# Performance work log

Hardware: AMD Instinct MI355X
Metric: run time of the kernel (lower is better)

## Reference

```python
import jax, jax.numpy as jnp
import numpy as np

N_NODES = 100000
N_EDGES = 3200000
N_GRAPHS = 128
IN_DIM = 4
HID = 64
BN_EPS = 1e-5


def setup_inputs() -> dict:
    key = jax.random.key(0)
    ks = jax.random.split(key, 24)
    x = jax.random.normal(ks[0], (N_NODES, IN_DIM), dtype=jnp.float32)
    edge_index = jax.random.randint(ks[1], (2, N_EDGES), 0, N_NODES, dtype=jnp.int32)
    batch_ids = jnp.sort(jax.random.randint(ks[2], (N_NODES,), 0, N_GRAPHS, dtype=jnp.int32))

    def lin(k, out_d, in_d):
        s = 1.0 / np.sqrt(in_d)
        return jax.random.uniform(k, (out_d, in_d), jnp.float32, -s, s)

    inp = {
        'x': x, 'edge_index': edge_index, 'batch_ids': batch_ids,
        # SAGEConv i: out = lin_l(mean_neighbors) + lin_r(x_self); bias lives in lin_l
        'w1l': lin(ks[3], HID, IN_DIM), 'b1': jnp.zeros((HID,), jnp.float32), 'w1r': lin(ks[4], HID, IN_DIM),
        'bn1_g': jnp.ones((HID,), jnp.float32), 'bn1_b': jnp.zeros((HID,), jnp.float32),
        'w2l': lin(ks[5], HID, HID), 'b2': jnp.zeros((HID,), jnp.float32), 'w2r': lin(ks[6], HID, HID),
        'bn2_g': jnp.ones((HID,), jnp.float32), 'bn2_b': jnp.zeros((HID,), jnp.float32),
        'w3l': lin(ks[7], HID, HID), 'b3': jnp.zeros((HID,), jnp.float32), 'w3r': lin(ks[8], HID, HID),
        'bn3_g': jnp.ones((HID,), jnp.float32), 'bn3_b': jnp.zeros((HID,), jnp.float32),
        'fc1_w': lin(ks[9], 64, HID), 'fc1_b': jnp.zeros((64,), jnp.float32),
        'fc2_w': lin(ks[10], 2, 64), 'fc2_b': jnp.zeros((2,), jnp.float32),
    }
    return inp


def _sage(x, src, dst, deg_inv, wl, bl, wr):
    # mean-aggregate neighbor messages (source -> target), then two small GEMMs
    msum = jax.ops.segment_sum(x[src], dst, num_segments=N_NODES)  # [N, d]
    agg = msum * deg_inv[:, None]
    return agg @ wl.T + bl + x @ wr.T


def _bn(x, g, b):
    # BatchNorm1d in training mode: batch stats over node dim, biased variance
    m = jnp.mean(x, axis=0)
    v = jnp.mean((x - m) ** 2, axis=0)
    return (x - m) * jax.lax.rsqrt(v + BN_EPS) * g + b


def reference(x, edge_index, batch_ids,
              w1l, b1, w1r, bn1_g, bn1_b,
              w2l, b2, w2r, bn2_g, bn2_b,
              w3l, b3, w3r, bn3_g, bn3_b,
              fc1_w, fc1_b, fc2_w, fc2_b):
    src, dst = edge_index[0], edge_index[1]
    deg = jax.ops.segment_sum(jnp.ones((src.shape[0],), x.dtype), dst, num_segments=N_NODES)
    deg_inv = 1.0 / jnp.maximum(deg, 1.0)

    h = jax.nn.relu(_bn(_sage(x, src, dst, deg_inv, w1l, b1, w1r), bn1_g, bn1_b))
    h = jax.nn.relu(_bn(_sage(h, src, dst, deg_inv, w2l, b2, w2r), bn2_g, bn2_b))
    h = jax.nn.relu(_bn(_sage(h, src, dst, deg_inv, w3l, b3, w3r), bn3_g, bn3_b))

    # global_mean_pool over graphs
    gsum = jax.ops.segment_sum(h, batch_ids, num_segments=N_GRAPHS)
    gcnt = jax.ops.segment_sum(jnp.ones((h.shape[0],), h.dtype), batch_ids, num_segments=N_GRAPHS)
    pooled = gsum / jnp.maximum(gcnt, 1.0)[:, None]

    # MLP head (dropout = identity at inference)
    hid = jax.nn.relu(pooled @ fc1_w.T + fc1_b)
    return hid @ fc2_w.T + fc2_b
```

## Files before the change

kernel.cpp:

```cpp
#include <hip/hip_runtime.h>
#include <hip/hip_fp16.h>

#define NN 100000
#define NE 3200000
#define NG 128
#define BN_EPS 1e-5f

#define NBUK 782
#define BSHIFT 7
#define BCAP 6144

#define GRID_SG 1024
#define PBMAX 2048
#define PSLICE 8

typedef _Float16 h2v __attribute__((ext_vector_type(2)));
typedef unsigned int u32x2 __attribute__((ext_vector_type(2)));
typedef unsigned int u32x4 __attribute__((ext_vector_type(4)));

static __device__ __forceinline__ h2v as_h2(unsigned int u) {
    return __builtin_bit_cast(h2v, u);
}
static __device__ __forceinline__ unsigned int as_u32(h2v h) {
    return __builtin_bit_cast(unsigned int, h);
}


__global__ void __launch_bounds__(512) k_scatter(
    const int* __restrict__ src, const int* __restrict__ dst,
    int* __restrict__ slab_cursor, unsigned int* __restrict__ slab, int E) {
    __shared__ int hist[NBUK + 2];
    __shared__ int cbase[NBUK + 2];
    int tid = threadIdx.x;
    int eBeg = blockIdx.x * 12500;
    int eEnd = min(eBeg + 12500, E);

    for (int t = tid; t < NBUK; t += 512) hist[t] = 0;
    __syncthreads();
    for (int e = eBeg + tid; e < eEnd; e += 512) {
        int b = dst[e] >> BSHIFT;
        atomicAdd(&hist[b], 1);
    }
    __syncthreads();
    for (int t = tid; t < NBUK; t += 512) {
        int c = hist[t];
        cbase[t] = (c > 0) ? atomicAdd(&slab_cursor[t], c) : 0;
    }
    __syncthreads();
    for (int t = tid; t < NBUK; t += 512) hist[t] = 0;
    __syncthreads();
    for (int e = eBeg + tid; e < eEnd; e += 512) {
        int d = dst[e];
        int b = d >> BSHIFT;
        int r = atomicAdd(&hist[b], 1);
        int pos = cbase[b] + r;
        if (pos < BCAP) slab[(size_t)b * BCAP + pos] = ((unsigned)src[e] << BSHIFT) | (unsigned)(d & 127);
    }
}

__global__ void __launch_bounds__(512) k_bucket_csr(
    const unsigned int* __restrict__ slab, const int* __restrict__ slab_cursor,
    int* __restrict__ row_ptr,
    float* __restrict__ deg_inv, int* __restrict__ csr_src,
    const float* __restrict__ x, const float* __restrict__ w1l,
    const float* __restrict__ b1, const float* __restrict__ w1r,
    __half* __restrict__ hp16, float* __restrict__ part) {
    __shared__ int lds_csr[BCAP];
    __shared__ int red[512];
    __shared__ int sdeg[128];
    __shared__ int sscan[128];
    __shared__ int slcur[128];
    __shared__ float swl[256], swr[256], sb1[64];
    __shared__ float ssum[64], ssq[64];
    int tid = threadIdx.x;
    int b = blockIdx.x;
    int lo = b << BSHIFT;
    int cnt = min(slab_cursor[b], BCAP);
    const unsigned int* sl = slab + (size_t)b * BCAP;

    int partial = 0;
    for (int j = tid; j < b; j += 512) partial += min(slab_cursor[j], BCAP);
    red[tid] = partial;
    __syncthreads();
    for (int off = 256; off > 0; off >>= 1) {
        if (tid < off) red[tid] += red[tid + off];
        __syncthreads();
    }
    int base = red[0];
    if (b == NBUK - 1 && tid == 0) row_ptr[NN] = base + cnt;

    if (tid < 256) { swl[tid] = w1l[tid]; swr[tid] = w1r[tid]; }
    if (tid < 64)  { sb1[tid] = b1[tid]; ssum[tid] = 0.f; ssq[tid] = 0.f; }
    if (tid < 128) sdeg[tid] = 0;
    __syncthreads();

    unsigned int myv[12];
    int mycount = 0;
    for (int k = tid; k < cnt; k += 512) myv[mycount++] = sl[k];
#pragma unroll
    for (int j = 0; j < 12; j++)
        if (j < mycount) atomicAdd(&sdeg[myv[j] & 127], 1);
    __syncthreads();
    int v = (tid < 128) ? sdeg[tid] : 0;
    if (tid < 128) sscan[tid] = v;
    __syncthreads();
    for (int off = 1; off < 128; off <<= 1) {
        int add = 0;
        if (tid < 128 && tid >= off) add = sscan[tid - off];
        __syncthreads();
        if (tid < 128) sscan[tid] += add;
        __syncthreads();
    }
    if (tid < 128) {
        int excl = sscan[tid] - v;
        int n = lo + tid;
        if (n < NN) {
            row_ptr[n] = base + excl;
            deg_inv[n] = 1.0f / fmaxf((float)v, 1.0f);
        }
        slcur[tid] = excl;
    }
    __syncthreads();
#pragma unroll
    for (int j = 0; j < 12; j++)
        if (j < mycount) {
            unsigned int p = myv[j];
            int pos = atomicAdd(&slcur[p & 127], 1);
            lds_csr[pos] = (int)(p >> BSHIFT);
        }
    __syncthreads();
    for (int k = tid; k < cnt; k += 512) csr_src[base + k] = lds_csr[k];

    int i = tid >> 2, c = tid & 3;
    int n = lo + i;
    bool valid = (n < NN);
    int dhi = sscan[i];
    int dlo = dhi - sdeg[i];
    const float4* x4 = (const float4*)x;
    float4 acc = make_float4(0.f, 0.f, 0.f, 0.f);
    int k = dlo + c;
    for (; k + 12 < dhi; k += 16) {
        int s0 = lds_csr[k], s1 = lds_csr[k + 4], s2 = lds_csr[k + 8], s3 = lds_csr[k + 12];
        float4 v0 = x4[s0];
        float4 v1 = x4[s1];
        float4 v2 = x4[s2];
        float4 v3 = x4[s3];
        acc.x += v0.x + v1.x + v2.x + v3.x;
        acc.y += v0.y + v1.y + v2.y + v3.y;
        acc.z += v0.z + v1.z + v2.z + v3.z;
        acc.w += v0.w + v1.w + v2.w + v3.w;
    }
    for (; k < dhi; k += 4) {
        int s = lds_csr[k];
        float4 xv = x4[s];
        acc.x += xv.x; acc.y += xv.y; acc.z += xv.z; acc.w += xv.w;
    }
#pragma unroll
    for (int m = 1; m <= 2; m <<= 1) {
        acc.x += __shfl_xor(acc.x, m);
        acc.y += __shfl_xor(acc.y, m);
        acc.z += __shfl_xor(acc.z, m);
        acc.w += __shfl_xor(acc.w, m);
    }
    float dv = 1.0f / fmaxf((float)sdeg[i], 1.0f);
    float ax = acc.x * dv, ay = acc.y * dv, az = acc.z * dv, aw = acc.w * dv;
    float4 xs = valid ? x4[n] : make_float4(0.f, 0.f, 0.f, 0.f);

#pragma unroll
    for (int m4 = 0; m4 < 4; m4++) {
        float4 o = make_float4(0.f, 0.f, 0.f, 0.f);
        float* op = &o.x;
        if (valid) {
#pragma unroll
            for (int t = 0; t < 4; t++) {
                int j = c * 16 + m4 * 4 + t;
                float s = sb1[j];
                s += ax * swl[j * 4 + 0] + ay * swl[j * 4 + 1] + az * swl[j * 4 + 2] + aw * swl[j * 4 + 3];
                s += xs.x * swr[j * 4 + 0] + xs.y * swr[j * 4 + 1] + xs.z * swr[j * 4 + 2] + xs.w * swr[j * 4 + 3];
                op[t] = s;
            }
            h2v p0 = h2v{(_Float16)o.x, (_Float16)o.y};
            h2v p1 = h2v{(_Float16)o.z, (_Float16)o.w};
            u32x2 w;
            w.x = *(unsigned int*)&p0;
            w.y = *(unsigned int*)&p1;
            __builtin_nontemporal_store(w, (u32x2*)hp16 + (size_t)n * 16 + c * 4 + m4);
        }
        float4 q = make_float4(o.x * o.x, o.y * o.y, o.z * o.z, o.w * o.w);
#pragma unroll
        for (int m = 4; m <= 32; m <<= 1) {
            o.x += __shfl_xor(o.x, m); o.y += __shfl_xor(o.y, m);
            o.z += __shfl_xor(o.z, m); o.w += __shfl_xor(o.w, m);
            q.x += __shfl_xor(q.x, m); q.y += __shfl_xor(q.y, m);
            q.z += __shfl_xor(q.z, m); q.w += __shfl_xor(q.w, m);
        }
        if ((tid & 63) < 4) {
            int jb = c * 16 + m4 * 4;
            atomicAdd(&ssum[jb + 0], o.x); atomicAdd(&ssum[jb + 1], o.y);
            atomicAdd(&ssum[jb + 2], o.z); atomicAdd(&ssum[jb + 3], o.w);
            atomicAdd(&ssq[jb + 0], q.x);  atomicAdd(&ssq[jb + 1], q.y);
            atomicAdd(&ssq[jb + 2], q.z);  atomicAdd(&ssq[jb + 3], q.w);
        }
    }
    __syncthreads();
    if (tid < 64) {
        part[(2 * tid) * PBMAX + blockIdx.x]     = ssum[tid];
        part[(2 * tid + 1) * PBMAX + blockIdx.x] = ssq[tid];
    }
}

__global__ void __launch_bounds__(256) k_bnact(
    const __half* __restrict__ hp, const float* __restrict__ sbv,
    __half* __restrict__ ha) {
    __shared__ float s_sc[64], s_bi[64];
    int tid = threadIdx.x;
    if (tid < 64) { s_sc[tid] = sbv[tid]; s_bi[tid] = sbv[64 + tid]; }
    __syncthreads();
    int c = tid & 7;
    h2v sc[4], bi[4];
#pragma unroll
    for (int j = 0; j < 4; j++) {
        sc[j] = h2v{(_Float16)s_sc[8 * c + 2 * j], (_Float16)s_sc[8 * c + 2 * j + 1]};
        bi[j] = h2v{(_Float16)s_bi[8 * c + 2 * j], (_Float16)s_bi[8 * c + 2 * j + 1]};
    }
    h2v hz = h2v{(_Float16)0.f, (_Float16)0.f};
    const u32x4* in4 = (const u32x4*)hp;
    u32x4* out4 = (u32x4*)ha;
    const int total = NN * 8;
    for (int i = blockIdx.x * 256 + tid; i < total; i += gridDim.x * 256) {
        u32x4 v = in4[i];
#pragma unroll
        for (int j = 0; j < 4; j++) {
            h2v a = as_h2(v[j]);
            a = __builtin_elementwise_max(a * sc[j] + bi[j], hz);
            v[j] = as_u32(a);
        }
        out4[i] = v;
    }
}

__global__ void __launch_bounds__(512, 8) k_sage(
    const __half* __restrict__ h_act,
    const int* __restrict__ row_ptr,
    const int* __restrict__ csr_src, const float* __restrict__ deg_inv,
    const float* __restrict__ wl, const float* __restrict__ bl,
    const float* __restrict__ wr, __half* __restrict__ hp16,
    float* __restrict__ part) {
    __shared__ h2v wl2s[32][68];
    __shared__ h2v wr2s[32][68];
    __shared__ h2v tAh[32][36];
    __shared__ h2v tXh[32][36];
    __shared__ float ssum[64], ssq[64];
    int tid = threadIdx.x;
    for (int idx = tid; idx < 2048; idx += 512) {
        int j = idx & 63, kk = idx >> 6;
        float2 l = ((const float2*)wl)[j * 32 + kk];
        float2 r = ((const float2*)wr)[j * 32 + kk];
        wl2s[kk][j] = h2v{(_Float16)l.x, (_Float16)l.y};
        wr2s[kk][j] = h2v{(_Float16)r.x, (_Float16)r.y};
    }
    if (tid < 64) { ssum[tid] = 0.f; ssq[tid] = 0.f; }
    __syncthreads();

    int g = tid & 15, ni = tid >> 4;
    unsigned g8 = (unsigned)(g << 3);
    h2v hz = h2v{(_Float16)0.f, (_Float16)0.f};
    const char* hb = (const char*)h_act;
    const int ntiles = NN / 32;
    float4 bo = ((const float4*)bl)[g];

    for (int tile = blockIdx.x; tile < ntiles; tile += GRID_SG) {
        int n = (tile << 5) + ni;
        int r0 = row_ptr[n], r1 = row_ptr[n + 1];
        float di = deg_inv[n];
        uint2 rsv = *(const uint2*)(hb + (((unsigned)n << 7) | g8));
        float ax = 0.f, ay = 0.f, az = 0.f, aw = 0.f;
        int e = r0;
        for (; e + 8 <= r1; e += 8) {
            int s0 = csr_src[e],     s1 = csr_src[e + 1], s2 = csr_src[e + 2], s3 = csr_src[e + 3];
            int s4 = csr_src[e + 4], s5 = csr_src[e + 5], s6 = csr_src[e + 6], s7 = csr_src[e + 7];
            uint2 v0 = *(const uint2*)(hb + (((unsigned)s0 << 7) | g8));
            uint2 v1 = *(const uint2*)(hb + (((unsigned)s1 << 7) | g8));
            uint2 v2 = *(const uint2*)(hb + (((unsigned)s2 << 7) | g8));
            uint2 v3 = *(const uint2*)(hb + (((unsigned)s3 << 7) | g8));
            uint2 v4 = *(const uint2*)(hb + (((unsigned)s4 << 7) | g8));
            uint2 v5 = *(const uint2*)(hb + (((unsigned)s5 << 7) | g8));
            uint2 v6 = *(const uint2*)(hb + (((unsigned)s6 << 7) | g8));
            uint2 v7 = *(const uint2*)(hb + (((unsigned)s7 << 7) | g8));
            h2v hacc0 = hz, hacc1 = hz;
            hacc0 += as_h2(v0.x); hacc1 += as_h2(v0.y);
            hacc0 += as_h2(v1.x); hacc1 += as_h2(v1.y);
            hacc0 += as_h2(v2.x); hacc1 += as_h2(v2.y);
            hacc0 += as_h2(v3.x); hacc1 += as_h2(v3.y);
            hacc0 += as_h2(v4.x); hacc1 += as_h2(v4.y);
            hacc0 += as_h2(v5.x); hacc1 += as_h2(v5.y);
            hacc0 += as_h2(v6.x); hacc1 += as_h2(v6.y);
            hacc0 += as_h2(v7.x); hacc1 += as_h2(v7.y);
            ax += (float)hacc0.x; ay += (float)hacc0.y;
            az += (float)hacc1.x; aw += (float)hacc1.y;
        }
        for (; e < r1; ++e) {
            int s = csr_src[e];
            uint2 vv = *(const uint2*)(hb + (((unsigned)s << 7) | g8));
            h2v a0 = as_h2(vv.x), a1 = as_h2(vv.y);
            ax += (float)a0.x; ay += (float)a0.y; az += (float)a1.x; aw += (float)a1.y;
        }
        ax *= di; ay *= di; az *= di; aw *= di;
        tAh[ni][2 * g]     = h2v{(_Float16)ax, (_Float16)ay};
        tAh[ni][2 * g + 1] = h2v{(_Float16)az, (_Float16)aw};
        tXh[ni][2 * g]     = as_h2(rsv.x);
        tXh[ni][2 * g + 1] = as_h2(rsv.y);
        __syncthreads();

        float4 o = bo;
#pragma unroll
        for (int kk = 0; kk < 32; kk += 4) {
            u32x4 av = *(const u32x4*)&tAh[ni][kk];
            u32x4 xv = *(const u32x4*)&tXh[ni][kk];
#pragma unroll
            for (int j = 0; j < 4; j++) {
                u32x4 wlv = *(const u32x4*)&wl2s[kk + j][4 * g];
                u32x4 wrv = *(const u32x4*)&wr2s[kk + j][4 * g];
                h2v a2 = as_h2(av[j]);
                h2v x2 = as_h2(xv[j]);
#if __has_builtin(__builtin_amdgcn_fdot2)
                o.x = __builtin_amdgcn_fdot2(a2, as_h2(wlv[0]), o.x, false);
                o.y = __builtin_amdgcn_fdot2(a2, as_h2(wlv[1]), o.y, false);
                o.z = __builtin_amdgcn_fdot2(a2, as_h2(wlv[2]), o.z, false);
                o.w = __builtin_amdgcn_fdot2(a2, as_h2(wlv[3]), o.w, false);
                o.x = __builtin_amdgcn_fdot2(x2, as_h2(wrv[0]), o.x, false);
                o.y = __builtin_amdgcn_fdot2(x2, as_h2(wrv[1]), o.y, false);
                o.z = __builtin_amdgcn_fdot2(x2, as_h2(wrv[2]), o.z, false);
                o.w = __builtin_amdgcn_fdot2(x2, as_h2(wrv[3]), o.w, false);
#else
                {
                    h2v l0 = as_h2(wlv[0]), l1 = as_h2(wlv[1]), l2 = as_h2(wlv[2]), l3 = as_h2(wlv[3]);
                    h2v q0 = as_h2(wrv[0]), q1 = as_h2(wrv[1]), q2 = as_h2(wrv[2]), q3 = as_h2(wrv[3]);
                    float b0 = (float)a2.x, b1 = (float)a2.y, x0 = (float)x2.x, x1 = (float)x2.y;
                    o.x += b0 * (float)l0.x + b1 * (float)l0.y + x0 * (float)q0.x + x1 * (float)q0.y;
                    o.y += b0 * (float)l1.x + b1 * (float)l1.y + x0 * (float)q1.x + x1 * (float)q1.y;
                    o.z += b0 * (float)l2.x + b1 * (float)l2.y + x0 * (float)q2.x + x1 * (float)q2.y;
                    o.w += b0 * (float)l3.x + b1 * (float)l3.y + x0 * (float)q3.x + x1 * (float)q3.y;
                }
#endif
            }
        }
        {
            h2v p0 = h2v{(_Float16)o.x, (_Float16)o.y};
            h2v p1 = h2v{(_Float16)o.z, (_Float16)o.w};
            u32x2 w;
            w.x = *(unsigned int*)&p0;
            w.y = *(unsigned int*)&p1;
            __builtin_nontemporal_store(w, (u32x2*)hp16 + (size_t)n * 16 + g);
        }

        float4 qv = make_float4(o.x * o.x, o.y * o.y, o.z * o.z, o.w * o.w);
#pragma unroll
        for (int m = 16; m <= 32; m <<= 1) {
            o.x += __shfl_xor(o.x, m); o.y += __shfl_xor(o.y, m);
            o.z += __shfl_xor(o.z, m); o.w += __shfl_xor(o.w, m);
            qv.x += __shfl_xor(qv.x, m); qv.y += __shfl_xor(qv.y, m);
            qv.z += __shfl_xor(qv.z, m); qv.w += __shfl_xor(qv.w, m);
        }
        if ((tid & 48) == 0) {
            atomicAdd(&ssum[4 * g + 0], o.x); atomicAdd(&ssum[4 * g + 1], o.y);
            atomicAdd(&ssum[4 * g + 2], o.z); atomicAdd(&ssum[4 * g + 3], o.w);
            atomicAdd(&ssq[4 * g + 0], qv.x);  atomicAdd(&ssq[4 * g + 1], qv.y);
            atomicAdd(&ssq[4 * g + 2], qv.z);  atomicAdd(&ssq[4 * g + 3], qv.w);
        }
        __syncthreads();
    }
    if (tid < 64) {
        part[(2 * tid) * PBMAX + blockIdx.x]     = ssum[tid];
        part[(2 * tid + 1) * PBMAX + blockIdx.x] = ssq[tid];
    }
}

__global__ void k_reduce_sb(const float* __restrict__ part, int PB,
                            const float* __restrict__ gamma, const float* __restrict__ beta,
                            float* __restrict__ sbv, int N) {
    int c = blockIdx.x;
    float s = 0.f, q = 0.f;
    for (int b = threadIdx.x; b < PB; b += 256) {
        s += part[(2 * c) * PBMAX + b];
        q += part[(2 * c + 1) * PBMAX + b];
    }
    __shared__ float rs[256], rq[256];
    rs[threadIdx.x] = s;
    rq[threadIdx.x] = q;
    __syncthreads();
    for (int off = 128; off > 0; off >>= 1) {
        if (threadIdx.x < off) {
            rs[threadIdx.x] += rs[threadIdx.x + off];
            rq[threadIdx.x] += rq[threadIdx.x + off];
        }
        __syncthreads();
    }
    if (threadIdx.x == 0) {
        float m = rs[0] / (float)N;
        float var = rq[0] / (float)N - m * m;
        float sc = gamma[c] * rsqrtf(var + BN_EPS);
        sbv[c]      = sc;
        sbv[64 + c] = beta[c] - m * sc;
    }
}

__global__ void __launch_bounds__(256) k_pool_partial(
    const __half* __restrict__ hp16, const float* __restrict__ sbv,
    const int* __restrict__ batch, float* __restrict__ pooled_part, int N) {
    __shared__ float ssc[64], sbi[64];
    __shared__ float sm[256];
    if (threadIdx.x < 64) {
        ssc[threadIdx.x] = sbv[threadIdx.x];
        sbi[threadIdx.x] = sbv[64 + threadIdx.x];
    }
    __syncthreads();
    int gph = blockIdx.x >> 3;
    int slice = blockIdx.x & 7;
    int lo = 0, hi = N;
    while (lo < hi) { int mid = (lo + hi) >> 1; if (batch[mid] < gph) lo = mid + 1; else hi = mid; }
    int start = lo;
    hi = N;
    while (lo < hi) { int mid = (lo + hi) >> 1; if (batch[mid] < gph + 1) lo = mid + 1; else hi = mid; }
    int end = lo;

    int c = threadIdx.x & 63, w = threadIdx.x >> 6;
    float s = 0.f;
    for (int r = start + slice * 4 + w; r < end; r += 32)
        s += fmaxf(__half2float(hp16[(size_t)r * 64 + c]) * ssc[c] + sbi[c], 0.f);
    sm[threadIdx.x] = s;
    __syncthreads();
    if (threadIdx.x < 64) {
        float t = sm[c] + sm[64 + c] + sm[128 + c] + sm[192 + c];
        pooled_part[(size_t)(gph * PSLICE + slice) * 64 + c] = t;
    }
}

__global__ void __launch_bounds__(64) k_head(
    const float* __restrict__ pooled_part, const int* __restrict__ batch,
    const float* __restrict__ fc1w, const float* __restrict__ fc1b,
    const float* __restrict__ fc2w, const float* __restrict__ fc2b,
    float* __restrict__ out, int N) {
    __shared__ float pl[64], hid[64];
    int gph = blockIdx.x;
    int j = threadIdx.x;
    int lo = 0, hi = N;
    while (lo < hi) { int mid = (lo + hi) >> 1; if (batch[mid] < gph) lo = mid + 1; else hi = mid; }
    int start = lo;
    hi = N;
    while (lo < hi) { int mid = (lo + hi) >> 1; if (batch[mid] < gph + 1) lo = mid + 1; else hi = mid; }
    int cnt = lo - start;

    float t = 0.f;
#pragma unroll
    for (int s = 0; s < PSLICE; s++) t += pooled_part[(size_t)(gph * PSLICE + s) * 64 + j];
    pl[j] = t / fmaxf((float)cnt, 1.0f);
    __syncthreads();
    float v = fc1b[j];
    for (int k = 0; k < 64; k++) v += pl[k] * fc1w[j * 64 + k];
    hid[j] = fmaxf(v, 0.f);
    __syncthreads();
    if (j < 2) {
        float o = fc2b[j];
        for (int k = 0; k < 64; k++) o += hid[k] * fc2w[j * 64 + k];
        out[gph * 2 + j] = o;
    }
}

extern "C" void kernel_launch(void* const* d_in, const int* in_sizes, int n_in,
                              void* d_out, int out_size, void* d_ws, size_t ws_size,
                              hipStream_t stream) {
    const float* x    = (const float*)d_in[0];
    const int* ei     = (const int*)d_in[1];
    const int* batch  = (const int*)d_in[2];
    const float* w1l  = (const float*)d_in[3];
    const float* b1   = (const float*)d_in[4];
    const float* w1r  = (const float*)d_in[5];
    const float* bn1g = (const float*)d_in[6];
    const float* bn1b = (const float*)d_in[7];
    const float* w2l  = (const float*)d_in[8];
    const float* b2   = (const float*)d_in[9];
    const float* w2r  = (const float*)d_in[10];
    const float* bn2g = (const float*)d_in[11];
    const float* bn2b = (const float*)d_in[12];
    const float* w3l  = (const float*)d_in[13];
    const float* b3   = (const float*)d_in[14];
    const float* w3r  = (const float*)d_in[15];
    const float* bn3g = (const float*)d_in[16];
    const float* bn3b = (const float*)d_in[17];
    const float* fc1w = (const float*)d_in[18];
    const float* fc1b = (const float*)d_in[19];
    const float* fc2w = (const float*)d_in[20];
    const float* fc2b = (const float*)d_in[21];
    float* out = (float*)d_out;

    const int N = NN, E = NE;
    const int* srcp = ei;
    const int* dstp = ei + E;

    char* ws = (char*)d_ws;
    size_t off = 0;
    auto alloc = [&](size_t bytes) -> char* {
        char* p = ws + off;
        off += (bytes + 255) & ~(size_t)255;
        return p;
    };
    int* csr_src       = (int*)alloc(sizeof(int) * E);
    __half* hpA        = (__half*)alloc(sizeof(__half) * N * 64);
    __half* hpB        = (__half*)alloc(sizeof(__half) * N * 64);
    unsigned int* slab = (unsigned int*)alloc(sizeof(unsigned int) * (size_t)NBUK * BCAP);
    int* slab_cursor   = (int*)alloc(sizeof(int) * NBUK);
    int* row_ptr       = (int*)alloc(sizeof(int) * (N + 1));
    float* deg_inv     = (float*)alloc(sizeof(float) * N);
    float* part        = (float*)alloc(sizeof(float) * 128 * PBMAX);
    float* sbv         = (float*)alloc(sizeof(float) * 128);
    float* pooled_part = (float*)alloc(sizeof(float) * NG * PSLICE * 64);

    __half* hAct = (__half*)slab;

    hipMemsetAsync(slab_cursor, 0, sizeof(int) * NBUK, stream);

    k_scatter<<<256, 512, 0, stream>>>(srcp, dstp, slab_cursor, slab, E);
    k_bucket_csr<<<NBUK, 512, 0, stream>>>(slab, slab_cursor, row_ptr, deg_inv,
                                           csr_src, x, w1l, b1, w1r, hpA, part);
    k_reduce_sb<<<64, 256, 0, stream>>>(part, NBUK, bn1g, bn1b, sbv, N);

    k_bnact<<<1024, 256, 0, stream>>>(hpA, sbv, hAct);
    k_sage<<<GRID_SG, 512, 0, stream>>>(hAct, row_ptr, csr_src, deg_inv,
                                        w2l, b2, w2r, hpB, part);
    k_reduce_sb<<<64, 256, 0, stream>>>(part, GRID_SG, bn2g, bn2b, sbv, N);

    k_bnact<<<1024, 256, 0, stream>>>(hpB, sbv, hAct);
    k_sage<<<GRID_SG, 512, 0, stream>>>(hAct, row_ptr, csr_src, deg_inv,
                                        w3l, b3, w3r, hpA, part);
    k_reduce_sb<<<64, 256, 0, stream>>>(part, GRID_SG, bn3g, bn3b, sbv, N);

    k_pool_partial<<<NG * PSLICE, 256, 0, stream>>>(hpA, sbv, batch, pooled_part, N);
    k_head<<<NG, 64, 0, stream>>>(pooled_part, batch, fc1w, fc1b, fc2w, fc2b, out, N);
}
```

Measured before the change: 390.0 us.

## Split neighbor gather across two thread teams with dynamic tile scheduling in SAGE

```diff
diff --git a/kernel.cpp b/kernel.cpp
--- a/kernel.cpp
+++ b/kernel.cpp
@@ -245,12 +245,14 @@
     const int* __restrict__ csr_src, const float* __restrict__ deg_inv,
     const float* __restrict__ wl, const float* __restrict__ bl,
     const float* __restrict__ wr, __half* __restrict__ hp16,
-    float* __restrict__ part) {
+    float* __restrict__ part, int* __restrict__ wctr) {
     __shared__ h2v wl2s[32][68];
     __shared__ h2v wr2s[32][68];
-    __shared__ h2v tAh[32][36];
+    __shared__ h2v tT0[32][36];
+    __shared__ h2v tT1[32][36];
     __shared__ h2v tXh[32][36];
     __shared__ float ssum[64], ssq[64];
+    __shared__ int stile;
     int tid = threadIdx.x;
     for (int idx = tid; idx < 2048; idx += 512) {
         int j = idx & 63, kk = idx >> 6;
@@ -262,66 +264,96 @@
     if (tid < 64) { ssum[tid] = 0.f; ssq[tid] = 0.f; }
     __syncthreads();
 
-    int g = tid & 15, ni = tid >> 4;
-    unsigned g8 = (unsigned)(g << 3);
+    int g = tid & 7;
+    int ni = (tid >> 3) & 31;
+    int team = tid >> 8;
+    unsigned g16 = (unsigned)(g << 4);
+    int g2 = tid & 15, ni2 = tid >> 4;
     h2v hz = h2v{(_Float16)0.f, (_Float16)0.f};
     const char* hb = (const char*)h_act;
     const int ntiles = NN / 32;
-    float4 bo = ((const float4*)bl)[g];
-
-    for (int tile = blockIdx.x; tile < ntiles; tile += GRID_SG) {
+    float4 bo = ((const float4*)bl)[g2];
+
+    int tile = blockIdx.x;
+    while (true) {
         int n = (tile << 5) + ni;
         int r0 = row_ptr[n], r1 = row_ptr[n + 1];
         float di = deg_inv[n];
-        uint2 rsv = *(const uint2*)(hb + (((unsigned)n << 7) | g8));
-        float ax = 0.f, ay = 0.f, az = 0.f, aw = 0.f;
-        int e = r0;
-        for (; e + 8 <= r1; e += 8) {
+        u32x4 rsv;
+        if (team == 0) rsv = *(const u32x4*)(hb + (((unsigned)n << 7) | g16));
+        int len = r1 - r0;
+        int h0 = (((len + 1) >> 1) + 7) & ~7;
+        if (h0 > len) h0 = len;
+        int e    = team ? (r0 + h0) : r0;
+        int eEnd = team ? r1 : (r0 + h0);
+
+        float f0 = 0.f, f1 = 0.f, f2 = 0.f, f3 = 0.f;
+        float f4 = 0.f, f5 = 0.f, f6 = 0.f, f7 = 0.f;
+        for (; e + 8 <= eEnd; e += 8) {
             int s0 = csr_src[e],     s1 = csr_src[e + 1], s2 = csr_src[e + 2], s3 = csr_src[e + 3];
             int s4 = csr_src[e + 4], s5 = csr_src[e + 5], s6 = csr_src[e + 6], s7 = csr_src[e + 7];
-            uint2 v0 = *(const uint2*)(hb + (((unsigned)s0 << 7) | g8));
-            uint2 v1 = *(const uint2*)(hb + (((unsigned)s1 << 7) | g8));
-            uint2 v2 = *(const uint2*)(hb + (((unsigned)s2 << 7) | g8));
-            uint2 v3 = *(const uint2*)(hb + (((unsigned)s3 << 7) | g8));
-            uint2 v4 = *(const uint2*)(hb + (((unsigned)s4 << 7) | g8));
-            uint2 v5 = *(const uint2*)(hb + (((unsigned)s5 << 7) | g8));
-            uint2 v6 = *(const uint2*)(hb + (((unsigned)s6 << 7) | g8));
-            uint2 v7 = *(const uint2*)(hb + (((unsigned)s7 << 7) | g8));
-            h2v hacc0 = hz, hacc1 = hz;
-            hacc0 += as_h2(v0.x); hacc1 += as_h2(v0.y);
-            hacc0 += as_h2(v1.x); hacc1 += as_h2(v1.y);
-            hacc0 += as_h2(v2.x); hacc1 += as_h2(v2.y);
-            hacc0 += as_h2(v3.x); hacc1 += as_h2(v3.y);
-            hacc0 += as_h2(v4.x); hacc1 += as_h2(v4.y);
-            hacc0 += as_h2(v5.x); hacc1 += as_h2(v5.y);
-            hacc0 += as_h2(v6.x); hacc1 += as_h2(v6.y);
-            hacc0 += as_h2(v7.x); hacc1 += as_h2(v7.y);
-            ax += (float)hacc0.x; ay += (float)hacc0.y;
-            az += (float)hacc1.x; aw += (float)hacc1.y;
-        }
-        for (; e < r1; ++e) {
-            int s = csr_src[e];
-            uint2 vv = *(const uint2*)(hb + (((unsigned)s << 7) | g8));
-            h2v a0 = as_h2(vv.x), a1 = as_h2(vv.y);
-            ax += (float)a0.x; ay += (float)a0.y; az += (float)a1.x; aw += (float)a1.y;
-        }
-        ax *= di; ay *= di; az *= di; aw *= di;
-        tAh[ni][2 * g]     = h2v{(_Float16)ax, (_Float16)ay};
-        tAh[ni][2 * g + 1] = h2v{(_Float16)az, (_Float16)aw};
-        tXh[ni][2 * g]     = as_h2(rsv.x);
-        tXh[ni][2 * g + 1] = as_h2(rsv.y);
+            u32x4 v0 = *(const u32x4*)(hb + (((unsigned)s0 << 7) | g16));
+            u32x4 v1 = *(const u32x4*)(hb + (((unsigned)s1 << 7) | g16));
+            u32x4 v2 = *(const u32x4*)(hb + (((unsigned)s2 << 7) | g16));
+            u32x4 v3 = *(const u32x4*)(hb + (((unsigned)s3 << 7) | g16));
+            u32x4 v4 = *(const u32x4*)(hb + (((unsigned)s4 << 7) | g16));
+            u32x4 v5 = *(const u32x4*)(hb + (((unsigned)s5 << 7) | g16));
+            u32x4 v6 = *(const u32x4*)(hb + (((unsigned)s6 << 7) | g16));
+            u32x4 v7 = *(const u32x4*)(hb + (((unsigned)s7 << 7) | g16));
+            h2v a0 = hz, a1 = hz, a2 = hz, a3 = hz;
+            a0 += as_h2(v0[0]); a1 += as_h2(v0[1]); a2 += as_h2(v0[2]); a3 += as_h2(v0[3]);
+            a0 += as_h2(v1[0]); a1 += as_h2(v1[1]); a2 += as_h2(v1[2]); a3 += as_h2(v1[3]);
+            a0 += as_h2(v2[0]); a1 += as_h2(v2[1]); a2 += as_h2(v2[2]); a3 += as_h2(v2[3]);
+            a0 += as_h2(v3[0]); a1 += as_h2(v3[1]); a2 += as_h2(v3[2]); a3 += as_h2(v3[3]);
+            a0 += as_h2(v4[0]); a1 += as_h2(v4[1]); a2 += as_h2(v4[2]); a3 += as_h2(v4[3]);
+            a0 += as_h2(v5[0]); a1 += as_h2(v5[1]); a2 += as_h2(v5[2]); a3 += as_h2(v5[3]);
+            a0 += as_h2(v6[0]); a1 += as_h2(v6[1]); a2 += as_h2(v6[2]); a3 += as_h2(v6[3]);
+            a0 += as_h2(v7[0]); a1 += as_h2(v7[1]); a2 += as_h2(v7[2]); a3 += as_h2(v7[3]);
+            f0 += (float)a0.x; f1 += (float)a0.y; f2 += (float)a1.x; f3 += (float)a1.y;
+            f4 += (float)a2.x; f5 += (float)a2.y; f6 += (float)a3.x; f7 += (float)a3.y;
+        }
+        {
+            h2v a0 = hz, a1 = hz, a2 = hz, a3 = hz;
+            for (; e < eEnd; ++e) {
+                int s = csr_src[e];
+                u32x4 vv = *(const u32x4*)(hb + (((unsigned)s << 7) | g16));
+                a0 += as_h2(vv[0]); a1 += as_h2(vv[1]); a2 += as_h2(vv[2]); a3 += as_h2(vv[3]);
+            }
+            f0 += (float)a0.x; f1 += (float)a0.y; f2 += (float)a1.x; f3 += (float)a1.y;
+            f4 += (float)a2.x; f5 += (float)a2.y; f6 += (float)a3.x; f7 += (float)a3.y;
+        }
+        f0 *= di; f1 *= di; f2 *= di; f3 *= di;
+        f4 *= di; f5 *= di; f6 *= di; f7 *= di;
+        {
+            h2v p0 = h2v{(_Float16)f0, (_Float16)f1};
+            h2v p1 = h2v{(_Float16)f2, (_Float16)f3};
+            h2v p2 = h2v{(_Float16)f4, (_Float16)f5};
+            h2v p3 = h2v{(_Float16)f6, (_Float16)f7};
+            u32x4 st;
+            st[0] = as_u32(p0); st[1] = as_u32(p1); st[2] = as_u32(p2); st[3] = as_u32(p3);
+            if (team == 0) {
+                *(u32x4*)&tT0[ni][4 * g] = st;
+                *(u32x4*)&tXh[ni][4 * g] = rsv;
+            } else {
+                *(u32x4*)&tT1[ni][4 * g] = st;
+            }
+        }
         __syncthreads();
 
+        if (tid == 0) stile = GRID_SG + atomicAdd(wctr, 1);
+
+        int n2 = (tile << 5) + ni2;
         float4 o = bo;
 #pragma unroll
         for (int kk = 0; kk < 32; kk += 4) {
-            u32x4 av = *(const u32x4*)&tAh[ni][kk];
-            u32x4 xv = *(const u32x4*)&tXh[ni][kk];
+            u32x4 a0v = *(const u32x4*)&tT0[ni2][kk];
+            u32x4 a1v = *(const u32x4*)&tT1[ni2][kk];
+            u32x4 xv  = *(const u32x4*)&tXh[ni2][kk];
 #pragma unroll
             for (int j = 0; j < 4; j++) {
-                u32x4 wlv = *(const u32x4*)&wl2s[kk + j][4 * g];
-                u32x4 wrv = *(const u32x4*)&wr2s[kk + j][4 * g];
-                h2v a2 = as_h2(av[j]);
+                u32x4 wlv = *(const u32x4*)&wl2s[kk + j][4 * g2];
+                u32x4 wrv = *(const u32x4*)&wr2s[kk + j][4 * g2];
+                h2v a2 = as_h2(a0v[j]) + as_h2(a1v[j]);
                 h2v x2 = as_h2(xv[j]);
 #if __has_builtin(__builtin_amdgcn_fdot2)
                 o.x = __builtin_amdgcn_fdot2(a2, as_h2(wlv[0]), o.x, false);
@@ -351,7 +383,7 @@
             u32x2 w;
             w.x = *(unsigned int*)&p0;
             w.y = *(unsigned int*)&p1;
-            __builtin_nontemporal_store(w, (u32x2*)hp16 + (size_t)n * 16 + g);
+            __builtin_nontemporal_store(w, (u32x2*)hp16 + (size_t)n2 * 16 + g2);
         }
 
         float4 qv = make_float4(o.x * o.x, o.y * o.y, o.z * o.z, o.w * o.w);
@@ -363,12 +395,14 @@
             qv.z += __shfl_xor(qv.z, m); qv.w += __shfl_xor(qv.w, m);
         }
         if ((tid & 48) == 0) {
-            atomicAdd(&ssum[4 * g + 0], o.x); atomicAdd(&ssum[4 * g + 1], o.y);
-            atomicAdd(&ssum[4 * g + 2], o.z); atomicAdd(&ssum[4 * g + 3], o.w);
-            atomicAdd(&ssq[4 * g + 0], qv.x);  atomicAdd(&ssq[4 * g + 1], qv.y);
-            atomicAdd(&ssq[4 * g + 2], qv.z);  atomicAdd(&ssq[4 * g + 3], qv.w);
+            atomicAdd(&ssum[4 * g2 + 0], o.x); atomicAdd(&ssum[4 * g2 + 1], o.y);
+            atomicAdd(&ssum[4 * g2 + 2], o.z); atomicAdd(&ssum[4 * g2 + 3], o.w);
+            atomicAdd(&ssq[4 * g2 + 0], qv.x);  atomicAdd(&ssq[4 * g2 + 1], qv.y);
+            atomicAdd(&ssq[4 * g2 + 2], qv.z);  atomicAdd(&ssq[4 * g2 + 3], qv.w);
         }
         __syncthreads();
+        tile = stile;
+        if (tile >= ntiles) break;
     }
     if (tid < 64) {
         part[(2 * tid) * PBMAX + blockIdx.x]     = ssum[tid];
@@ -515,10 +549,12 @@
     float* part        = (float*)alloc(sizeof(float) * 128 * PBMAX);
     float* sbv         = (float*)alloc(sizeof(float) * 128);
     float* pooled_part = (float*)alloc(sizeof(float) * NG * PSLICE * 64);
+    int* wctr          = (int*)alloc(sizeof(int) * 2);
 
     __half* hAct = (__half*)slab;
 
     hipMemsetAsync(slab_cursor, 0, sizeof(int) * NBUK, stream);
+    hipMemsetAsync(wctr, 0, sizeof(int) * 2, stream);
 
     k_scatter<<<256, 512, 0, stream>>>(srcp, dstp, slab_cursor, slab, E);
     k_bucket_csr<<<NBUK, 512, 0, stream>>>(slab, slab_cursor, row_ptr, deg_inv,
@@ -527,12 +563,12 @@
 
     k_bnact<<<1024, 256, 0, stream>>>(hpA, sbv, hAct);
     k_sage<<<GRID_SG, 512, 0, stream>>>(hAct, row_ptr, csr_src, deg_inv,
-                                        w2l, b2, w2r, hpB, part);
+                                        w2l, b2, w2r, hpB, part, wctr);
     k_reduce_sb<<<64, 256, 0, stream>>>(part, GRID_SG, bn2g, bn2b, sbv, N);
 
     k_bnact<<<1024, 256, 0, stream>>>(hpB, sbv, hAct);
     k_sage<<<GRID_SG, 512, 0, stream>>>(hAct, row_ptr, csr_src, deg_inv,
-                                        w3l, b3, w3r, hpA, part);
+                                        w3l, b3, w3r, hpA, part, wctr + 1);
     k_reduce_sb<<<64, 256, 0, stream>>>(part, GRID_SG, bn3g, bn3b, sbv, N);
 
     k_pool_partial<<<NG * PSLICE, 256, 0, stream>>>(hpA, sbv, batch, pooled_part, N);
```

New measurement: 411.9 us. 1.06x slower.

## Use atomic work-stealing tile scheduler in SAGE kernel and deepen gather unroll

Applied to the files above, without the earlier changes.

```diff
diff --git a/kernel.cpp b/kernel.cpp
--- a/kernel.cpp
+++ b/kernel.cpp
@@ -10,7 +10,7 @@
 #define BSHIFT 7
 #define BCAP 6144
 
-#define GRID_SG 1024
+#define GRID_SG 768
 #define PBMAX 2048
 #define PSLICE 8
 
@@ -239,18 +239,19 @@
     }
 }
 
-__global__ void __launch_bounds__(512, 8) k_sage(
+__global__ void __launch_bounds__(512, 6) k_sage(
     const __half* __restrict__ h_act,
     const int* __restrict__ row_ptr,
     const int* __restrict__ csr_src, const float* __restrict__ deg_inv,
     const float* __restrict__ wl, const float* __restrict__ bl,
     const float* __restrict__ wr, __half* __restrict__ hp16,
-    float* __restrict__ part) {
+    float* __restrict__ part, int* __restrict__ wctr) {
     __shared__ h2v wl2s[32][68];
     __shared__ h2v wr2s[32][68];
     __shared__ h2v tAh[32][36];
     __shared__ h2v tXh[32][36];
     __shared__ float ssum[64], ssq[64];
+    __shared__ int stile;
     int tid = threadIdx.x;
     for (int idx = tid; idx < 2048; idx += 512) {
         int j = idx & 63, kk = idx >> 6;
@@ -269,14 +270,59 @@
     const int ntiles = NN / 32;
     float4 bo = ((const float4*)bl)[g];
 
-    for (int tile = blockIdx.x; tile < ntiles; tile += GRID_SG) {
+    int tile = blockIdx.x;
+    while (true) {
         int n = (tile << 5) + ni;
         int r0 = row_ptr[n], r1 = row_ptr[n + 1];
         float di = deg_inv[n];
         uint2 rsv = *(const uint2*)(hb + (((unsigned)n << 7) | g8));
         float ax = 0.f, ay = 0.f, az = 0.f, aw = 0.f;
         int e = r0;
-        for (; e + 8 <= r1; e += 8) {
+        for (; e + 16 <= r1; e += 16) {
+            int s0 = csr_src[e],      s1 = csr_src[e + 1],  s2 = csr_src[e + 2],  s3 = csr_src[e + 3];
+            int s4 = csr_src[e + 4],  s5 = csr_src[e + 5],  s6 = csr_src[e + 6],  s7 = csr_src[e + 7];
+            int s8 = csr_src[e + 8],  s9 = csr_src[e + 9],  sa = csr_src[e + 10], sb = csr_src[e + 11];
+            int sc = csr_src[e + 12], sd = csr_src[e + 13], se = csr_src[e + 14], sf = csr_src[e + 15];
+            uint2 v0 = *(const uint2*)(hb + (((unsigned)s0 << 7) | g8));
+            uint2 v1 = *(const uint2*)(hb + (((unsigned)s1 << 7) | g8));
+            uint2 v2 = *(const uint2*)(hb + (((unsigned)s2 << 7) | g8));
+            uint2 v3 = *(const uint2*)(hb + (((unsigned)s3 << 7) | g8));
+            uint2 v4 = *(const uint2*)(hb + (((unsigned)s4 << 7) | g8));
+            uint2 v5 = *(const uint2*)(hb + (((unsigned)s5 << 7) | g8));
+            uint2 v6 = *(const uint2*)(hb + (((unsigned)s6 << 7) | g8));
+            uint2 v7 = *(const uint2*)(hb + (((unsigned)s7 << 7) | g8));
+            uint2 v8 = *(const uint2*)(hb + (((unsigned)s8 << 7) | g8));
+            uint2 v9 = *(const uint2*)(hb + (((unsigned)s9 << 7) | g8));
+            uint2 va = *(const uint2*)(hb + (((unsigned)sa << 7) | g8));
+            uint2 vb = *(const uint2*)(hb + (((unsigned)sb << 7) | g8));
+            uint2 vc = *(const uint2*)(hb + (((unsigned)sc << 7) | g8));
+            uint2 vd = *(const uint2*)(hb + (((unsigned)sd << 7) | g8));
+            uint2 ve = *(const uint2*)(hb + (((unsigned)se << 7) | g8));
+            uint2 vf = *(const uint2*)(hb + (((unsigned)sf << 7) | g8));
+            h2v hacc0 = hz, hacc1 = hz;
+            hacc0 += as_h2(v0.x); hacc1 += as_h2(v0.y);
+            hacc0 += as_h2(v1.x); hacc1 += as_h2(v1.y);
+            hacc0 += as_h2(v2.x); hacc1 += as_h2(v2.y);
+            hacc0 += as_h2(v3.x); hacc1 += as_h2(v3.y);
+            hacc0 += as_h2(v4.x); hacc1 += as_h2(v4.y);
+            hacc0 += as_h2(v5.x); hacc1 += as_h2(v5.y);
+            hacc0 += as_h2(v6.x); hacc1 += as_h2(v6.y);
+            hacc0 += as_h2(v7.x); hacc1 += as_h2(v7.y);
+            ax += (float)hacc0.x; ay += (float)hacc0.y;
+            az += (float)hacc1.x; aw += (float)hacc1.y;
+            hacc0 = hz; hacc1 = hz;
+            hacc0 += as_h2(v8.x); hacc1 += as_h2(v8.y);
+            hacc0 += as_h2(v9.x); hacc1 += as_h2(v9.y);
+            hacc0 += as_h2(va.x); hacc1 += as_h2(va.y);
+            hacc0 += as_h2(vb.x); hacc1 += as_h2(vb.y);
+            hacc0 += as_h2(vc.x); hacc1 += as_h2(vc.y);
+            hacc0 += as_h2(vd.x); hacc1 += as_h2(vd.y);
+            hacc0 += as_h2(ve.x); hacc1 += as_h2(ve.y);
+            hacc0 += as_h2(vf.x); hacc1 += as_h2(vf.y);
+            ax += (float)hacc0.x; ay += (float)hacc0.y;
+            az += (float)hacc1.x; aw += (float)hacc1.y;
+        }
+        if (e + 8 <= r1) {
             int s0 = csr_src[e],     s1 = csr_src[e + 1], s2 = csr_src[e + 2], s3 = csr_src[e + 3];
             int s4 = csr_src[e + 4], s5 = csr_src[e + 5], s6 = csr_src[e + 6], s7 = csr_src[e + 7];
             uint2 v0 = *(const uint2*)(hb + (((unsigned)s0 << 7) | g8));
@@ -298,6 +344,7 @@
             hacc0 += as_h2(v7.x); hacc1 += as_h2(v7.y);
             ax += (float)hacc0.x; ay += (float)hacc0.y;
             az += (float)hacc1.x; aw += (float)hacc1.y;
+            e += 8;
         }
         for (; e < r1; ++e) {
             int s = csr_src[e];
@@ -311,6 +358,8 @@
         tXh[ni][2 * g]     = as_h2(rsv.x);
         tXh[ni][2 * g + 1] = as_h2(rsv.y);
         __syncthreads();
+
+        if (tid == 0) stile = GRID_SG + atomicAdd(wctr, 1);
 
         float4 o = bo;
 #pragma unroll
@@ -369,6 +418,8 @@
             atomicAdd(&ssq[4 * g + 2], qv.z);  atomicAdd(&ssq[4 * g + 3], qv.w);
         }
         __syncthreads();
+        tile = stile;
+        if (tile >= ntiles) break;
     }
     if (tid < 64) {
         part[(2 * tid) * PBMAX + blockIdx.x]     = ssum[tid];
@@ -510,6 +561,7 @@
     __half* hpB        = (__half*)alloc(sizeof(__half) * N * 64);
     unsigned int* slab = (unsigned int*)alloc(sizeof(unsigned int) * (size_t)NBUK * BCAP);
     int* slab_cursor   = (int*)alloc(sizeof(int) * NBUK);
+    int* wctr          = (int*)alloc(sizeof(int) * 2);
     int* row_ptr       = (int*)alloc(sizeof(int) * (N + 1));
     float* deg_inv     = (float*)alloc(sizeof(float) * N);
     float* part        = (float*)alloc(sizeof(float) * 128 * PBMAX);
@@ -518,7 +570,7 @@
 
     __half* hAct = (__half*)slab;
 
-    hipMemsetAsync(slab_cursor, 0, sizeof(int) * NBUK, stream);
+    hipMemsetAsync(slab_cursor, 0, ((sizeof(int) * NBUK + 255) & ~(size_t)255) + sizeof(int) * 2, stream);
 
     k_scatter<<<256, 512, 0, stream>>>(srcp, dstp, slab_cursor, slab, E);
     k_bucket_csr<<<NBUK, 512, 0, stream>>>(slab, slab_cursor, row_ptr, deg_inv,
@@ -527,12 +579,12 @@
 
     k_bnact<<<1024, 256, 0, stream>>>(hpA, sbv, hAct);
     k_sage<<<GRID_SG, 512, 0, stream>>>(hAct, row_ptr, csr_src, deg_inv,
-                                        w2l, b2, w2r, hpB, part);
+                                        w2l, b2, w2r, hpB, part, wctr);
     k_reduce_sb<<<64, 256, 0, stream>>>(part, GRID_SG, bn2g, bn2b, sbv, N);
 
     k_bnact<<<1024, 256, 0, stream>>>(hpB, sbv, hAct);
     k_sage<<<GRID_SG, 512, 0, stream>>>(hAct, row_ptr, csr_src, deg_inv,
-                                        w3l, b3, w3r, hpA, part);
+                                        w3l, b3, w3r, hpA, part, wctr + 1);
     k_reduce_sb<<<64, 256, 0, stream>>>(part, GRID_SG, bn3g, bn3b, sbv, N);
 
     k_pool_partial<<<NG * PSLICE, 256, 0, stream>>>(hpA, sbv, batch, pooled_part, N);
```

Result: slower. 398.2 us (+2.1%).
